# Kernel optimization log

Measured on AMD Instinct MI355X. Metric: run time of the kernel, lower is better.

The kernel has to match this reference:

```python
import jax, jax.numpy as jnp
import numpy as np

B = 8192       # number of windows (batch*windows_per_image)
N = 49         # tokens per 7x7 window
C = 128        # channels
H = 4          # heads
HD = C // H    # head dim = 32
WIN = (7, 7)


def _relative_position_index(win):
    wh, ww = win
    coords = np.stack(np.meshgrid(np.arange(wh), np.arange(ww), indexing='ij'))
    cf = coords.reshape(2, -1)                       # (2, N)
    rel = (cf[:, :, None] - cf[:, None, :]).transpose(1, 2, 0)  # (N, N, 2)
    rel[:, :, 0] += wh - 1
    rel[:, :, 1] += ww - 1
    rel[:, :, 0] *= 2 * ww - 1
    return jnp.array(rel.sum(-1).reshape(-1), dtype=jnp.int32)  # (N*N,)


def setup_inputs() -> dict:
    key = jax.random.key(0)
    ks = jax.random.split(key, 7)
    x = jax.random.normal(ks[0], (B, N, C), dtype=jnp.float32)
    mask = jax.random.normal(ks[1], (B, 1, N, N), dtype=jnp.float32)
    qkv_w = jax.random.normal(ks[2], (C, 3 * C), dtype=jnp.float32) * (C ** -0.5)
    qkv_b = jnp.zeros((3 * C,), dtype=jnp.float32)
    rel_bias_table = jax.random.normal(ks[3], ((2 * WIN[0] - 1) * (2 * WIN[1] - 1), H), dtype=jnp.float32)
    proj_w = jax.random.normal(ks[4], (C, C), dtype=jnp.float32) * (C ** -0.5)
    proj_b = jnp.zeros((C,), dtype=jnp.float32)
    rel_index = _relative_position_index(WIN)
    return {"x": x, "mask": mask, "qkv_w": qkv_w, "qkv_b": qkv_b,
            "rel_bias_table": rel_bias_table, "proj_w": proj_w,
            "proj_b": proj_b, "rel_index": rel_index}


def reference(x, mask, qkv_w, qkv_b, rel_bias_table, proj_w, proj_b, rel_index):
    b, n, c = x.shape
    scale = HD ** -0.5
    qkv = (x @ qkv_w + qkv_b).reshape(b, n, 3, H, HD).transpose(2, 0, 3, 1, 4)
    q, k, v = qkv[0] * scale, qkv[1], qkv[2]          # (b, H, n, HD)
    attn = jnp.einsum('bhqd,bhkd->bhqk', q, k)        # (b, H, n, n)
    # gathered relative position bias: (n*n, H) -> (1, H, n, n)
    bias = rel_bias_table[rel_index].reshape(n, n, H).transpose(2, 0, 1)[None]
    attn = jax.nn.softmax(attn + bias + mask, axis=-1)
    out = jnp.einsum('bhqk,bhkd->bhqd', attn, v)       # (b, H, n, HD)
    out = out.transpose(0, 2, 1, 3).reshape(b, n, c)
    return out @ proj_w + proj_b
```

## Files before the change

kernel.cpp:

```cpp
#include <hip/hip_runtime.h>
#include <hip/hip_bf16.h>

using f32x4 = __attribute__((ext_vector_type(4))) float;
using bf16x8 = __attribute__((ext_vector_type(8))) short;

#define DEVI __device__ __forceinline__

DEVI short f2bf(float f) { __hip_bfloat16 h = __float2bfloat16(f); return *reinterpret_cast<short*>(&h); }
DEVI unsigned int pk2(float a, float b) {
    float2 t; t.x = a; t.y = b;
    __hip_bfloat162 h = __float22bfloat162_rn(t);
    return *reinterpret_cast<unsigned int*>(&h);
}
DEVI float bf2f(unsigned short s) { unsigned int u = ((unsigned int)s) << 16; return __uint_as_float(u); }

DEVI void pl32swap(unsigned& a, unsigned& b) { asm("v_permlane32_swap_b32 %0, %1" : "+v"(a), "+v"(b)); }
DEVI void pl16swap(unsigned& a, unsigned& b) { asm("v_permlane16_swap_b32 %0, %1" : "+v"(a), "+v"(b)); }

#define GLOAD_LDS16(gp, lp) \
    __builtin_amdgcn_global_load_lds((const __attribute__((address_space(1))) void*)(gp), \
                                     (__attribute__((address_space(3))) void*)(lp), 16, 0, 0)

constexpr int NB = 8192;
constexpr int NT = 49;
constexpr int CD = 128;
constexpr float SCALE = 0.17677669529663687f;
constexpr float LOG2E = 1.4426950408889634f;

constexpr size_t WS_QKVWT  = 0;
constexpr size_t WS_PROJWT = 98304;
constexpr size_t WS_BIAS   = 131072;
constexpr size_t WS_QKV    = 150528;
constexpr size_t SQKV      = (size_t)NB * 4 * NT * 32;

DEVI void div49(unsigned grow, unsigned& bI, unsigned& tI) {
    bI = (unsigned)(((unsigned long long)grow * 2804876602ull) >> 37);
    tI = grow - bI * 49u;
}

DEVI int swz128(int row, int col) { return row * 128 + (col ^ ((row & 7) << 3)); }

__global__ __launch_bounds__(256) void prep_kernel(
    const float* __restrict__ qkv_w, const float* __restrict__ proj_w,
    const float* __restrict__ rbt, const int* __restrict__ rel_index,
    short* __restrict__ qkvwS, short* __restrict__ projwT, unsigned short* __restrict__ biasBf)
{
    int i = blockIdx.x * 256 + threadIdx.x;
    if (i < 384 * 128) {
        int n = i >> 7, j = i & 127;
        int c = n >> 7, r = n & 127;
        qkvwS[c * 16384 + r * 128 + (j ^ ((r & 7) << 3))] = f2bf(qkv_w[j * 384 + n]);
    }
    if (i < 128 * 128) {
        int n = i >> 7, j = i & 127;
        projwT[n * 128 + j] = f2bf(proj_w[j * 128 + n]);
    }
    if (i < 4 * NT * NT) {
        int h = i / (NT * NT); int t = i % (NT * NT);
        int k = t / NT, q = t - k * NT;
        biasBf[i] = (unsigned short)f2bf(rbt[rel_index[q * NT + k] * 4 + h] * LOG2E);
    }
}

__global__ __launch_bounds__(256, 2) void qkv_gemm_kernel(
    const float* __restrict__ x, const float* __restrict__ qkv_b,
    const short* __restrict__ qkvwS, short* __restrict__ qkv)
{
    __shared__ short ldsB[16384];
    const int tid = threadIdx.x;
    const int w = tid >> 6, lane = tid & 63, lr = lane & 15, lg = lane >> 4;
    const unsigned m0 = blockIdx.x * 128 + w * 32;

    bf16x8 af[2][4];
#pragma unroll
    for (int mf = 0; mf < 2; ++mf) {
        const float* xrow = x + (size_t)(m0 + mf * 16 + lr) * CD;
#pragma unroll
        for (int kt = 0; kt < 4; ++kt) {
            const float4* p = reinterpret_cast<const float4*>(xrow + kt * 32 + lg * 8);
            float4 v0 = p[0], v1 = p[1];
            union { unsigned int u[4]; bf16x8 v; } cv;
            cv.u[0] = pk2(v0.x, v0.y); cv.u[1] = pk2(v0.z, v0.w);
            cv.u[2] = pk2(v1.x, v1.y); cv.u[3] = pk2(v1.z, v1.w);
            af[mf][kt] = cv.v;
        }
    }

    unsigned rowoff[2][4];
#pragma unroll
    for (int mf = 0; mf < 2; ++mf)
#pragma unroll
        for (int r = 0; r < 4; ++r) {
            unsigned bI, tI;
            div49(m0 + mf * 16 + 4 * lg + r, bI, tI);
            rowoff[mf][r] = bI * 6272u + tI * 32u;
        }

    const char* srcB = (const char*)qkvwS;
    char* ldsBc = (char*)ldsB;

#pragma unroll
    for (int c = 0; c < 3; ++c) {
#pragma unroll
        for (int i = 0; i < 8; ++i)
            GLOAD_LDS16(srcB + c * 32768 + w * 8192 + i * 1024 + lane * 16,
                        ldsBc + w * 8192 + i * 1024);
        __syncthreads();

        f32x4 acc[2][8];
#pragma unroll
        for (int mf = 0; mf < 2; ++mf)
#pragma unroll
            for (int n = 0; n < 8; ++n) acc[mf][n] = f32x4{0.f, 0.f, 0.f, 0.f};

#pragma unroll
        for (int ntl = 0; ntl < 8; ++ntl) {
            const int rrow = ntl * 16 + lr;
            const char* rbase = ldsBc + rrow * 256;
            const int sw = (lr & 7) << 4;
#pragma unroll
            for (int kt = 0; kt < 4; ++kt) {
                bf16x8 bb = *reinterpret_cast<const bf16x8*>(rbase + ((kt * 64 + lg * 16) ^ sw));
                acc[0][ntl] = __builtin_amdgcn_mfma_f32_16x16x32_bf16(af[0][kt], bb, acc[0][ntl], 0, 0, 0);
                acc[1][ntl] = __builtin_amdgcn_mfma_f32_16x16x32_bf16(af[1][kt], bb, acc[1][ntl], 0, 0, 0);
            }
        }

        const float scl = (c == 0) ? SCALE * LOG2E : 1.0f;
        short* dplane = qkv + (size_t)c * SQKV;
#pragma unroll
        for (int ntl = 0; ntl < 8; ++ntl) {
            const int h = ntl >> 1;
            const int d = (ntl & 1) * 16 + lr;
            const float bias = qkv_b[c * 128 + ntl * 16 + lr];
#pragma unroll
            for (int mf = 0; mf < 2; ++mf)
#pragma unroll
                for (int r = 0; r < 4; ++r)
                    dplane[rowoff[mf][r] + h * 1568 + d] = f2bf((acc[mf][ntl][r] + bias) * scl);
        }
        __syncthreads();
    }
}

__global__ __launch_bounds__(512, 4) void attn_proj_kernel(
    const short* __restrict__ qkv, const float* __restrict__ mask,
    const unsigned short* __restrict__ biasT, const short* __restrict__ projwT,
    const float* __restrict__ proj_b, float* __restrict__ out)
{
    __shared__ float mT[50 * 65];
    __shared__ short vS[4][2048];
    __shared__ short oS[64 * 128];

    const int b = blockIdx.x;
    const int tid = threadIdx.x;
    const int w = tid >> 6, lane = tid & 63, lr = lane & 15, lg = lane >> 4;
    const int h = w >> 1, half = w & 1;

    const size_t slice = (size_t)(b * 4 + h) * (NT * 32);
    const short* qg = qkv + slice;
    const short* kg = qkv + SQKV + slice;
    const short* vg = qkv + 2 * SQKV + slice;
    short* vSl = vS[h];

    bf16x8 bbf[4];
    {
        const short* brow = projwT + (w * 16 + lr) * 128 + lg * 8;
#pragma unroll
        for (int kt = 0; kt < 4; ++kt)
            bbf[kt] = *reinterpret_cast<const bf16x8*>(brow + kt * 32);
    }

    const int mt0 = 2 * half;
    bf16x8 qa[2], kb[4];
#pragma unroll
    for (int i = 0; i < 2; ++i)
        qa[i] = *reinterpret_cast<const bf16x8*>(qg + (16 * (mt0 + i) + lr) * 32 + lg * 8);
#pragma unroll
    for (int t4 = 0; t4 < 4; ++t4)
        kb[t4] = *reinterpret_cast<const bf16x8*>(kg + (16 * t4 + lr) * 32 + lg * 8);

    for (int i = tid; i < 50 * 65; i += 512) mT[i] = 0.f;

    const float* mb_ = mask + (size_t)b * (NT * NT);
    float mreg[5];
#pragma unroll
    for (int ii = 0; ii < 5; ++ii) {
        int i = tid + ii * 512;
        mreg[ii] = (i < NT * NT) ? mb_[i] * LOG2E : 0.f;
    }

    for (int ii = 0; ii < 4; ++ii) {
        int i = ii * 64 + lane;
        int tt = 32 * half + (i & 31);
        int d0 = (i >> 5) * 4;
        short4 v4 = {0, 0, 0, 0};
        if (tt < NT) v4 = *reinterpret_cast<const short4*>(vg + tt * 32 + d0);
        int a = tt >> 4, bb2 = tt & 15;
        int col = (bb2 < 8) ? (a * 8 + bb2) : (24 + a * 8 + bb2);
        vSl[(d0 + 0) * 64 + (col ^ (((d0 + 0) & 7) << 3))] = v4.x;
        vSl[(d0 + 1) * 64 + (col ^ (((d0 + 1) & 7) << 3))] = v4.y;
        vSl[(d0 + 2) * 64 + (col ^ (((d0 + 2) & 7) << 3))] = v4.z;
        vSl[(d0 + 3) * 64 + (col ^ (((d0 + 3) & 7) << 3))] = v4.w;
    }
    __syncthreads();

#pragma unroll
    for (int ii = 0; ii < 5; ++ii) {
        int i = tid + ii * 512;
        if (i < NT * NT) {
            unsigned q_, k_;
            div49((unsigned)i, q_, k_);
            mT[k_ * 65 + q_] = mreg[ii];
        }
    }
    __syncthreads();

    bf16x8 vb[2][2];
    const int sw8 = (lr & 7) << 3;
#pragma unroll
    for (int nt = 0; nt < 2; ++nt)
#pragma unroll
        for (int blk = 0; blk < 2; ++blk)
            vb[nt][blk] = *reinterpret_cast<const bf16x8*>(
                &vSl[(16 * nt + lr) * 64 + ((blk * 32 + 8 * lg) ^ sw8)]);

    const unsigned short* biasTh = biasT + h * (NT * NT);
    float mbb[2][4][4];
#pragma unroll
    for (int mt2 = 0; mt2 < 2; ++mt2) {
        const int qcol = 16 * (mt0 + mt2) + lr;
#pragma unroll
        for (int ct = 0; ct < 4; ++ct)
#pragma unroll
            for (int r = 0; r < 4; ++r) {
                int k = 16 * ct + 4 * lg + r;
                int kc = min(k, 49);
                mbb[mt2][ct][r] = mT[kc * 65 + qcol] + bf2f(biasTh[kc * NT + qcol]);
            }
    }

    f32x4 oacc[2][2];
#pragma unroll
    for (int mt2 = 0; mt2 < 2; ++mt2) { oacc[mt2][0] = f32x4{0,0,0,0}; oacc[mt2][1] = f32x4{0,0,0,0}; }

#pragma unroll
    for (int mt2 = 0; mt2 < 2; ++mt2) {
        f32x4 sacc[4];
#pragma unroll
        for (int ct = 0; ct < 4; ++ct) {
            f32x4 z = {0.f, 0.f, 0.f, 0.f};
            sacc[ct] = __builtin_amdgcn_mfma_f32_16x16x32_bf16(kb[ct], qa[mt2], z, 0, 0, 0);
        }

        float e[4][4];
        float psum = 0.f;
#pragma unroll
        for (int ct = 0; ct < 4; ++ct)
#pragma unroll
            for (int r = 0; r < 4; ++r) {
                float ee = exp2f(sacc[ct][r] + mbb[mt2][ct][r]);
                if (ct == 3) ee = (r == 0 && lg == 0) ? ee : 0.f;
                e[ct][r] = ee;
                psum += ee;
            }
        psum += __shfl_xor(psum, 16);
        psum += __shfl_xor(psum, 32);
        const float inv = 1.0f / psum;

        unsigned A0 = pk2(e[0][0] * inv, e[0][1] * inv);
        unsigned A1 = pk2(e[1][0] * inv, e[1][1] * inv);
        unsigned A2 = pk2(e[2][0] * inv, e[2][1] * inv);
        unsigned A3 = pk2(e[3][0] * inv, e[3][1] * inv);
        unsigned B0 = pk2(e[0][2] * inv, e[0][3] * inv);
        unsigned B1 = pk2(e[1][2] * inv, e[1][3] * inv);
        unsigned B2 = pk2(e[2][2] * inv, e[2][3] * inv);
        unsigned B3 = pk2(e[3][2] * inv, e[3][3] * inv);
        pl32swap(A0, A2); pl32swap(A1, A3);
        pl16swap(A0, A1); pl16swap(A2, A3);
        pl32swap(B0, B2); pl32swap(B1, B3);
        pl16swap(B0, B1); pl16swap(B2, B3);
        union { unsigned u[4]; bf16x8 v; } p0, p1;
        p0.u[0] = A0; p0.u[1] = B0; p0.u[2] = A1; p0.u[3] = B1;
        p1.u[0] = A2; p1.u[1] = B2; p1.u[2] = A3; p1.u[3] = B3;

#pragma unroll
        for (int nt = 0; nt < 2; ++nt) {
            oacc[mt2][nt] = __builtin_amdgcn_mfma_f32_16x16x32_bf16(p0.v, vb[nt][0], oacc[mt2][nt], 0, 0, 0);
            oacc[mt2][nt] = __builtin_amdgcn_mfma_f32_16x16x32_bf16(p1.v, vb[nt][1], oacc[mt2][nt], 0, 0, 0);
        }
    }

#pragma unroll
    for (int mt2 = 0; mt2 < 2; ++mt2)
#pragma unroll
        for (int nt = 0; nt < 2; ++nt)
#pragma unroll
            for (int r = 0; r < 4; ++r) {
                int row = 16 * (mt0 + mt2) + 4 * lg + r;
                int col = 32 * h + 16 * nt + lr;
                oS[swz128(row, col)] = f2bf(oacc[mt2][nt][r]);
            }
    __syncthreads();

    {
        f32x4 acc[4];
#pragma unroll
        for (int mf = 0; mf < 4; ++mf) acc[mf] = f32x4{0.f, 0.f, 0.f, 0.f};

#pragma unroll
        for (int mf = 0; mf < 4; ++mf) {
#pragma unroll
            for (int kt = 0; kt < 4; ++kt) {
                bf16x8 af = *reinterpret_cast<const bf16x8*>(&oS[swz128(16 * mf + lr, kt * 32 + lg * 8)]);
                acc[mf] = __builtin_amdgcn_mfma_f32_16x16x32_bf16(af, bbf[kt], acc[mf], 0, 0, 0);
            }
        }

        const int col = w * 16 + lr;
        const float pb = proj_b[col];
#pragma unroll
        for (int mf = 0; mf < 4; ++mf)
#pragma unroll
            for (int r = 0; r < 4; ++r) {
                int row = 16 * mf + 4 * lg + r;
                if (row < NT)
                    out[((size_t)b * NT + row) * CD + col] = acc[mf][r] + pb;
            }
    }
}

extern "C" void kernel_launch(void* const* d_in, const int* in_sizes, int n_in,
                              void* d_out, int out_size, void* d_ws, size_t ws_size,
                              hipStream_t stream) {
    const float* x      = (const float*)d_in[0];
    const float* mask   = (const float*)d_in[1];
    const float* qkv_w  = (const float*)d_in[2];
    const float* qkv_b  = (const float*)d_in[3];
    const float* rbt    = (const float*)d_in[4];
    const float* proj_w = (const float*)d_in[5];
    const float* proj_b = (const float*)d_in[6];
    const int*   ridx   = (const int*)d_in[7];
    float* out = (float*)d_out;

    char* ws = (char*)d_ws;
    short* qkvwS  = (short*)(ws + WS_QKVWT);
    short* projwT = (short*)(ws + WS_PROJWT);
    unsigned short* biasBf = (unsigned short*)(ws + WS_BIAS);
    short* qkv = (short*)(ws + WS_QKV);

    prep_kernel<<<192, 256, 0, stream>>>(qkv_w, proj_w, rbt, ridx, qkvwS, projwT, biasBf);
    qkv_gemm_kernel<<<(NB * NT) / 128, 256, 0, stream>>>(x, qkv_b, qkvwS, qkv);
    attn_proj_kernel<<<NB, 512, 0, stream>>>(qkv, mask, biasBf, projwT, proj_b, out);
}
```

Measured before the change: 312.8 us.

## Fuse QKV projection into attention kernel, keeping Q/K/V in LDS

Merges the separate QKV GEMM kernel into the per-window attention kernel. Each block computes its window's Q, K and V from x with MFMA and writes them straight into swizzled LDS buffers, so the bf16 QKV intermediate never goes to global memory and one launch is dropped. The trade-off is that every block now streams the full 96KB of QKV weights through LDS in three chunks, with extra barriers. Work is also spent on padded rows (64 rows for 49 tokens), and the larger LDS pool could reduce occupancy.

```diff
diff --git a/kernel.cpp b/kernel.cpp
--- a/kernel.cpp
+++ b/kernel.cpp
@@ -30,8 +30,6 @@
 constexpr size_t WS_QKVWT  = 0;
 constexpr size_t WS_PROJWT = 98304;
 constexpr size_t WS_BIAS   = 131072;
-constexpr size_t WS_QKV    = 150528;
-constexpr size_t SQKV      = (size_t)NB * 4 * NT * 32;
 
 DEVI void div49(unsigned grow, unsigned& bI, unsigned& tI) {
     bI = (unsigned)(((unsigned long long)grow * 2804876602ull) >> 37);
@@ -62,23 +60,44 @@
     }
 }
 
-__global__ __launch_bounds__(256, 2) void qkv_gemm_kernel(
-    const float* __restrict__ x, const float* __restrict__ qkv_b,
-    const short* __restrict__ qkvwS, short* __restrict__ qkv)
+__global__ __launch_bounds__(512, 4) void fused_kernel(
+    const float* __restrict__ x, const float* __restrict__ mask,
+    const float* __restrict__ qkv_b, const short* __restrict__ qkvwS,
+    const unsigned short* __restrict__ biasT, const short* __restrict__ projwT,
+    const float* __restrict__ proj_b, float* __restrict__ out)
 {
-    __shared__ short ldsB[16384];
+    __shared__ __attribute__((aligned(16))) short pool[40960];
+    short* qkL = pool;
+    short* vS  = pool + 16384;
+    char*  Wcb = (char*)(pool + 24576);
+    float* mT  = (float*)(pool + 24576);
+
+    const int b = blockIdx.x;
     const int tid = threadIdx.x;
     const int w = tid >> 6, lane = tid & 63, lr = lane & 15, lg = lane >> 4;
-    const unsigned m0 = blockIdx.x * 128 + w * 32;
+    const int h = w >> 1, half = w & 1;
+
+    const float* mb_ = mask + (size_t)b * (NT * NT);
+    float mreg[5];
+#pragma unroll
+    for (int ii = 0; ii < 5; ++ii) {
+        int i = tid + ii * 512;
+        mreg[ii] = (i < NT * NT) ? mb_[i] * LOG2E : 0.f;
+    }
 
     bf16x8 af[2][4];
 #pragma unroll
     for (int mf = 0; mf < 2; ++mf) {
-        const float* xrow = x + (size_t)(m0 + mf * 16 + lr) * CD;
+        const int row = 32 * (w & 1) + 16 * mf + lr;
+        const bool valid = row < NT;
+        const float* xrow = x + ((size_t)b * NT + (valid ? row : 0)) * CD;
 #pragma unroll
         for (int kt = 0; kt < 4; ++kt) {
-            const float4* p = reinterpret_cast<const float4*>(xrow + kt * 32 + lg * 8);
-            float4 v0 = p[0], v1 = p[1];
+            float4 v0 = {0.f,0.f,0.f,0.f}, v1 = {0.f,0.f,0.f,0.f};
+            if (valid) {
+                const float4* p = reinterpret_cast<const float4*>(xrow + kt * 32 + lg * 8);
+                v0 = p[0]; v1 = p[1];
+            }
             union { unsigned int u[4]; bf16x8 v; } cv;
             cv.u[0] = pk2(v0.x, v0.y); cv.u[1] = pk2(v0.z, v0.w);
             cv.u[2] = pk2(v1.x, v1.y); cv.u[3] = pk2(v1.z, v1.w);
@@ -86,125 +105,81 @@
         }
     }
 
-    unsigned rowoff[2][4];
-#pragma unroll
-    for (int mf = 0; mf < 2; ++mf)
-#pragma unroll
-        for (int r = 0; r < 4; ++r) {
-            unsigned bI, tI;
-            div49(m0 + mf * 16 + 4 * lg + r, bI, tI);
-            rowoff[mf][r] = bI * 6272u + tI * 32u;
-        }
-
-    const char* srcB = (const char*)qkvwS;
-    char* ldsBc = (char*)ldsB;
-
+    float biasr[3][2];
+#pragma unroll
+    for (int c = 0; c < 3; ++c)
+#pragma unroll
+        for (int nn = 0; nn < 2; ++nn)
+            biasr[c][nn] = qkv_b[(c * 8 + (w >> 1) + 4 * nn) * 16 + lr];
+
+    const char* srcW = (const char*)qkvwS;
 #pragma unroll
     for (int c = 0; c < 3; ++c) {
 #pragma unroll
-        for (int i = 0; i < 8; ++i)
-            GLOAD_LDS16(srcB + c * 32768 + w * 8192 + i * 1024 + lane * 16,
-                        ldsBc + w * 8192 + i * 1024);
+        for (int i = 0; i < 4; ++i)
+            GLOAD_LDS16(srcW + c * 32768 + w * 4096 + i * 1024 + lane * 16,
+                        Wcb + w * 4096 + i * 1024);
         __syncthreads();
 
-        f32x4 acc[2][8];
-#pragma unroll
-        for (int mf = 0; mf < 2; ++mf)
-#pragma unroll
-            for (int n = 0; n < 8; ++n) acc[mf][n] = f32x4{0.f, 0.f, 0.f, 0.f};
-
-#pragma unroll
-        for (int ntl = 0; ntl < 8; ++ntl) {
-            const int rrow = ntl * 16 + lr;
-            const char* rbase = ldsBc + rrow * 256;
-            const int sw = (lr & 7) << 4;
-#pragma unroll
-            for (int kt = 0; kt < 4; ++kt) {
-                bf16x8 bb = *reinterpret_cast<const bf16x8*>(rbase + ((kt * 64 + lg * 16) ^ sw));
-                acc[0][ntl] = __builtin_amdgcn_mfma_f32_16x16x32_bf16(af[0][kt], bb, acc[0][ntl], 0, 0, 0);
-                acc[1][ntl] = __builtin_amdgcn_mfma_f32_16x16x32_bf16(af[1][kt], bb, acc[1][ntl], 0, 0, 0);
-            }
-        }
-
-        const float scl = (c == 0) ? SCALE * LOG2E : 1.0f;
-        short* dplane = qkv + (size_t)c * SQKV;
-#pragma unroll
-        for (int ntl = 0; ntl < 8; ++ntl) {
-            const int h = ntl >> 1;
-            const int d = (ntl & 1) * 16 + lr;
-            const float bias = qkv_b[c * 128 + ntl * 16 + lr];
-#pragma unroll
-            for (int mf = 0; mf < 2; ++mf)
-#pragma unroll
-                for (int r = 0; r < 4; ++r)
-                    dplane[rowoff[mf][r] + h * 1568 + d] = f2bf((acc[mf][ntl][r] + bias) * scl);
+#pragma unroll
+        for (int nn = 0; nn < 2; ++nn) {
+            const int ntl = (w >> 1) + 4 * nn;
+            const int nt  = c * 8 + ntl;
+            const int s   = nt >> 3;
+            const int hh  = (nt >> 1) & 3;
+            const int d0  = (nt & 1) * 16;
+            const int d   = d0 + lr;
+            const float scl = (s == 0) ? SCALE * LOG2E : 1.0f;
+#pragma unroll
+            for (int mf = 0; mf < 2; ++mf) {
+                const int rt = 2 * (w & 1) + mf;
+                f32x4 acc = {0.f, 0.f, 0.f, 0.f};
+#pragma unroll
+                for (int kt = 0; kt < 4; ++kt) {
+                    bf16x8 bb = *reinterpret_cast<const bf16x8*>(
+                        Wcb + (ntl * 16 + lr) * 256 + ((kt * 64 + lg * 16) ^ ((lr & 7) << 4)));
+                    acc = __builtin_amdgcn_mfma_f32_16x16x32_bf16(af[mf][kt], bb, acc, 0, 0, 0);
+                }
+#pragma unroll
+                for (int r = 0; r < 4; ++r) {
+                    const int row = rt * 16 + 4 * lg + r;
+                    const short val = f2bf((acc[r] + biasr[c][nn]) * scl);
+                    if (s < 2) {
+                        const int g0 = s * 4 + (d >> 3);
+                        qkL[hh * 4096 + row * 64 + (((g0 ^ (row & 7)) << 3) | (d & 7))] = val;
+                    } else {
+                        const int a2 = row >> 4, bb2 = row & 15;
+                        const int col = (bb2 < 8) ? (a2 * 8 + bb2) : (24 + a2 * 8 + bb2);
+                        vS[hh * 2048 + d * 64 + (col ^ ((d & 7) << 3))] = val;
+                    }
+                }
+            }
         }
         __syncthreads();
     }
-}
-
-__global__ __launch_bounds__(512, 4) void attn_proj_kernel(
-    const short* __restrict__ qkv, const float* __restrict__ mask,
-    const unsigned short* __restrict__ biasT, const short* __restrict__ projwT,
-    const float* __restrict__ proj_b, float* __restrict__ out)
-{
-    __shared__ float mT[50 * 65];
-    __shared__ short vS[4][2048];
-    __shared__ short oS[64 * 128];
-
-    const int b = blockIdx.x;
-    const int tid = threadIdx.x;
-    const int w = tid >> 6, lane = tid & 63, lr = lane & 15, lg = lane >> 4;
-    const int h = w >> 1, half = w & 1;
-
-    const size_t slice = (size_t)(b * 4 + h) * (NT * 32);
-    const short* qg = qkv + slice;
-    const short* kg = qkv + SQKV + slice;
-    const short* vg = qkv + 2 * SQKV + slice;
-    short* vSl = vS[h];
-
-    bf16x8 bbf[4];
+
+    const int mt0 = 2 * half;
+    bf16x8 qa[2], kb[4], vb[2][2];
+#pragma unroll
+    for (int i = 0; i < 2; ++i) {
+        const int row = 16 * (mt0 + i) + lr;
+        qa[i] = *reinterpret_cast<const bf16x8*>(&qkL[h * 4096 + row * 64 + ((lg ^ (row & 7)) << 3)]);
+    }
+#pragma unroll
+    for (int t4 = 0; t4 < 4; ++t4) {
+        const int row = 16 * t4 + lr;
+        kb[t4] = *reinterpret_cast<const bf16x8*>(&qkL[h * 4096 + row * 64 + (((4 | lg) ^ (row & 7)) << 3)]);
+    }
     {
-        const short* brow = projwT + (w * 16 + lr) * 128 + lg * 8;
-#pragma unroll
-        for (int kt = 0; kt < 4; ++kt)
-            bbf[kt] = *reinterpret_cast<const bf16x8*>(brow + kt * 32);
-    }
-
-    const int mt0 = 2 * half;
-    bf16x8 qa[2], kb[4];
-#pragma unroll
-    for (int i = 0; i < 2; ++i)
-        qa[i] = *reinterpret_cast<const bf16x8*>(qg + (16 * (mt0 + i) + lr) * 32 + lg * 8);
-#pragma unroll
-    for (int t4 = 0; t4 < 4; ++t4)
-        kb[t4] = *reinterpret_cast<const bf16x8*>(kg + (16 * t4 + lr) * 32 + lg * 8);
-
-    for (int i = tid; i < 50 * 65; i += 512) mT[i] = 0.f;
-
-    const float* mb_ = mask + (size_t)b * (NT * NT);
-    float mreg[5];
-#pragma unroll
-    for (int ii = 0; ii < 5; ++ii) {
-        int i = tid + ii * 512;
-        mreg[ii] = (i < NT * NT) ? mb_[i] * LOG2E : 0.f;
-    }
-
-    for (int ii = 0; ii < 4; ++ii) {
-        int i = ii * 64 + lane;
-        int tt = 32 * half + (i & 31);
-        int d0 = (i >> 5) * 4;
-        short4 v4 = {0, 0, 0, 0};
-        if (tt < NT) v4 = *reinterpret_cast<const short4*>(vg + tt * 32 + d0);
-        int a = tt >> 4, bb2 = tt & 15;
-        int col = (bb2 < 8) ? (a * 8 + bb2) : (24 + a * 8 + bb2);
-        vSl[(d0 + 0) * 64 + (col ^ (((d0 + 0) & 7) << 3))] = v4.x;
-        vSl[(d0 + 1) * 64 + (col ^ (((d0 + 1) & 7) << 3))] = v4.y;
-        vSl[(d0 + 2) * 64 + (col ^ (((d0 + 2) & 7) << 3))] = v4.z;
-        vSl[(d0 + 3) * 64 + (col ^ (((d0 + 3) & 7) << 3))] = v4.w;
-    }
-    __syncthreads();
-
+        const short* vSl = vS + h * 2048;
+        const int sw8 = (lr & 7) << 3;
+#pragma unroll
+        for (int nt = 0; nt < 2; ++nt)
+#pragma unroll
+            for (int blk = 0; blk < 2; ++blk)
+                vb[nt][blk] = *reinterpret_cast<const bf16x8*>(
+                    &vSl[(16 * nt + lr) * 64 + ((blk * 32 + 8 * lg) ^ sw8)]);
+    }
 #pragma unroll
     for (int ii = 0; ii < 5; ++ii) {
         int i = tid + ii * 512;
@@ -215,15 +190,6 @@
         }
     }
     __syncthreads();
-
-    bf16x8 vb[2][2];
-    const int sw8 = (lr & 7) << 3;
-#pragma unroll
-    for (int nt = 0; nt < 2; ++nt)
-#pragma unroll
-        for (int blk = 0; blk < 2; ++blk)
-            vb[nt][blk] = *reinterpret_cast<const bf16x8*>(
-                &vSl[(16 * nt + lr) * 64 + ((blk * 32 + 8 * lg) ^ sw8)]);
 
     const unsigned short* biasTh = biasT + h * (NT * NT);
     float mbb[2][4][4];
@@ -291,6 +257,7 @@
         }
     }
 
+    short* oS = qkL;
 #pragma unroll
     for (int mt2 = 0; mt2 < 2; ++mt2)
 #pragma unroll
@@ -304,18 +271,23 @@
     __syncthreads();
 
     {
+        bf16x8 bbf[4];
+        const short* brow = projwT + (w * 16 + lr) * 128 + lg * 8;
+#pragma unroll
+        for (int kt = 0; kt < 4; ++kt)
+            bbf[kt] = *reinterpret_cast<const bf16x8*>(brow + kt * 32);
+
         f32x4 acc[4];
 #pragma unroll
         for (int mf = 0; mf < 4; ++mf) acc[mf] = f32x4{0.f, 0.f, 0.f, 0.f};
 
 #pragma unroll
-        for (int mf = 0; mf < 4; ++mf) {
+        for (int mf = 0; mf < 4; ++mf)
 #pragma unroll
             for (int kt = 0; kt < 4; ++kt) {
-                bf16x8 af = *reinterpret_cast<const bf16x8*>(&oS[swz128(16 * mf + lr, kt * 32 + lg * 8)]);
-                acc[mf] = __builtin_amdgcn_mfma_f32_16x16x32_bf16(af, bbf[kt], acc[mf], 0, 0, 0);
-            }
-        }
+                bf16x8 a2 = *reinterpret_cast<const bf16x8*>(&oS[swz128(16 * mf + lr, kt * 32 + lg * 8)]);
+                acc[mf] = __builtin_amdgcn_mfma_f32_16x16x32_bf16(a2, bbf[kt], acc[mf], 0, 0, 0);
+            }
 
         const int col = w * 16 + lr;
         const float pb = proj_b[col];
@@ -347,9 +319,7 @@
     short* qkvwS  = (short*)(ws + WS_QKVWT);
     short* projwT = (short*)(ws + WS_PROJWT);
     unsigned short* biasBf = (unsigned short*)(ws + WS_BIAS);
-    short* qkv = (short*)(ws + WS_QKV);
 
     prep_kernel<<<192, 256, 0, stream>>>(qkv_w, proj_w, rbt, ridx, qkvwS, projwT, biasBf);
-    qkv_gemm_kernel<<<(NB * NT) / 128, 256, 0, stream>>>(x, qkv_b, qkvwS, qkv);
-    attn_proj_kernel<<<NB, 512, 0, stream>>>(qkv, mask, biasBf, projwT, proj_b, out);
-}
+    fused_kernel<<<NB, 512, 0, stream>>>(x, mask, qkv_b, qkvwS, biasBf, projwT, proj_b, out);
+}
```

New measurement: 296.7 us. 1.05x faster.
